# Optimization experiments

Measured on AMD Instinct MI355X. Metric: run time of the kernel, lower is better.

Reference implementation:

```python
import jax, jax.numpy as jnp
import numpy as np

N, D, F, E, K = 8192, 1024, 4096, 8, 2


def setup_inputs() -> dict:
    key = jax.random.key(0)
    ks = jax.random.split(key, 4)
    x = jax.random.normal(ks[0], (N, D), dtype=jnp.float32)
    Wg = jax.random.normal(ks[1], (D, E), dtype=jnp.float32) * 0.02
    W1 = jax.random.normal(ks[2], (E, D, F), dtype=jnp.float32) * 0.02
    b1 = jnp.zeros((E, F), dtype=jnp.float32)
    W2 = jax.random.normal(ks[3], (E, F, D), dtype=jnp.float32) * 0.02
    b2 = jnp.zeros((E, D), dtype=jnp.float32)
    return {"x": x, "Wg": Wg, "W1": W1, "b1": b1, "W2": W2, "b2": b2}


def reference(x, Wg, W1, b1, W2, b2):
    # Top-k softmax gate (TopKGate): pick K experts per token, renormalize.
    logits = x @ Wg                                        # [N, E]
    probs = jax.nn.softmax(logits, axis=-1)
    gate_vals, expert_idx = jax.lax.top_k(probs, K)        # [N, K]
    gate_w = gate_vals / jnp.sum(gate_vals, axis=-1, keepdims=True)

    # Expert FFN (dispatch/combine math): the torch code sorts tokens by expert
    # id, all-to-alls them to the owning rank, applies the local Expert MLP,
    # and combines back weighted by gate_w. The jit-friendly equivalent is to
    # compute every expert's MLP for all tokens and gather the selected rows.
    h = jax.nn.relu(jnp.einsum('nd,edf->enf', x, W1) + b1[:, None, :])  # [E, N, F]
    o = jnp.einsum('enf,efd->end', h, W2) + b2[:, None, :]               # [E, N, D]

    tok = jnp.arange(x.shape[0])
    sel = o[expert_idx, tok[:, None]]                      # [N, K, D]
    y = jnp.sum(gate_w[..., None] * sel, axis=1)           # [N, D]
    return y
```

## Files before the change

kernel.cpp:

```cpp
#include <hip/hip_runtime.h>

#define N_TOK 8192
#define DIM   1024
#define FFN   4096
#define NEXP  8
#define TOPK  2
#define NENT  (N_TOK * TOPK)
#define MAXM  20

using short8   = __attribute__((ext_vector_type(8))) short;
using ushort8v = __attribute__((ext_vector_type(8))) unsigned short;
using floatx4  = __attribute__((ext_vector_type(4))) float;

__device__ __forceinline__ unsigned short f2bf(float f) {
    union { float f; unsigned u; } v; v.f = f;
    unsigned r = v.u + 0x7fffu + ((v.u >> 16) & 1u);
    return (unsigned short)(r >> 16);
}

#define GLOAD_LDS16(gptr, lptr) __builtin_amdgcn_global_load_lds( \
    (__attribute__((address_space(1))) void*)(void*)(gptr),       \
    (__attribute__((address_space(3))) void*)(lptr), 16, 0, 0)


__device__ __forceinline__ void transpose_tile(const float* __restrict__ inp,
                                               unsigned short* __restrict__ outp,
                                               int R, int C, int r0, int c0,
                                               float* __restrict__ tile) {
    int t = threadIdx.x;
    int p = t & 7;
    int trow = t >> 3;
    int w = t >> 6;
#pragma unroll
    for (int i = 0; i < 8; i++) {
        int r = i * 32 + trow;
        float4 v = *(const float4*)&inp[(size_t)(r0 + r) * C + c0 + p * 4];
        int cc = p ^ ((4 * i + w) & 7);
        *(float4*)&tile[r * 32 + cc * 4] = v;
    }
    __syncthreads();
    int c = t >> 3;
    int cbase = ((c >> 2) ^ p) * 4 + (c & 3);
    unsigned short* orow = outp + (size_t)(c0 + c) * R + r0;
#pragma unroll
    for (int j = 0; j < 4; j++) {
        int rb = j * 64 + p * 8;
        ushort8v us;
#pragma unroll
        for (int k = 0; k < 8; k++)
            us[k] = f2bf(tile[(rb + k) * 32 + cbase]);
        *(ushort8v*)&orow[rb] = us;
    }
}


__global__ __launch_bounds__(256) void prep_kernel(
    const float* __restrict__ W1, unsigned short* __restrict__ w1t,
    const float* __restrict__ x, const float* __restrict__ wg,
    unsigned short* __restrict__ xb,
    int* __restrict__ topk_e, float* __restrict__ topk_w,
    int* __restrict__ counts)
{
    __shared__ float tile[8192];
    int bid = blockIdx.x;
    if (bid < 4096) {
        int rt = bid & 3;
        int ct = (bid >> 2) & 127;
        int e  = bid >> 9;
        transpose_tile(W1 + (size_t)e * DIM * FFN, w1t + (size_t)e * DIM * FFN,
                       DIM, FFN, rt * 256, ct * 32, tile);
        return;
    }

    int tid = threadIdx.x;
    int wave = tid >> 6, lane = tid & 63;
    int t = (bid - 4096) * 4 + wave;
    const float* xr = x + (size_t)t * DIM;
    unsigned short* xbr = xb + (size_t)t * DIM;
    float acc[NEXP];
#pragma unroll
    for (int e = 0; e < NEXP; e++) acc[e] = 0.f;
    for (int it = 0; it < DIM / 256; it++) {
        int d = it * 256 + lane * 4;
        float4 xv = *(const float4*)&xr[d];
        ushort4 ub;
        ub.x = f2bf(xv.x); ub.y = f2bf(xv.y); ub.z = f2bf(xv.z); ub.w = f2bf(xv.w);
        *(ushort4*)&xbr[d] = ub;
        const float* wp = wg + (size_t)d * NEXP;
#pragma unroll
        for (int j = 0; j < 4; j++) {
            float xj = (j == 0) ? xv.x : (j == 1) ? xv.y : (j == 2) ? xv.z : xv.w;
            const float4* wr = (const float4*)(wp + j * NEXP);
            float4 w0 = wr[0], w1 = wr[1];
            acc[0] += xj * w0.x; acc[1] += xj * w0.y; acc[2] += xj * w0.z; acc[3] += xj * w0.w;
            acc[4] += xj * w1.x; acc[5] += xj * w1.y; acc[6] += xj * w1.z; acc[7] += xj * w1.w;
        }
    }
#pragma unroll
    for (int e = 0; e < NEXP; e++) {
#pragma unroll
        for (int off = 32; off > 0; off >>= 1) acc[e] += __shfl_xor(acc[e], off);
    }
    if (lane == 0) {
        int e1 = 0; float l1 = acc[0];
        for (int e = 1; e < NEXP; e++) if (acc[e] > l1) { l1 = acc[e]; e1 = e; }
        int e2 = -1; float l2 = -3.4e38f;
        for (int e = 0; e < NEXP; e++) if (e != e1 && acc[e] > l2) { l2 = acc[e]; e2 = e; }
        float w1v = 1.f / (1.f + expf(l2 - l1));
        topk_e[t * 2]     = e1;  topk_e[t * 2 + 1] = e2;
        topk_w[t * 2]     = w1v; topk_w[t * 2 + 1] = 1.f - w1v;
        atomicAdd(&counts[e1], 1);
        atomicAdd(&counts[e2], 1);
    }
}


__global__ __launch_bounds__(256) void scatter_kernel(const int* __restrict__ topk_e,
                                                      const float* __restrict__ topk_w,
                                                      const int* __restrict__ counts,
                                                      int* __restrict__ offs,
                                                      int* __restrict__ cursors,
                                                      int* __restrict__ entry_token,
                                                      float* __restrict__ entry_w,
                                                      float* __restrict__ y) {
    if (blockIdx.x >= 32) {
        float4 z = make_float4(0.f, 0.f, 0.f, 0.f);
        float4* yp = (float4*)y;
        size_t base = (size_t)(blockIdx.x - 32) * 256 + threadIdx.x;
#pragma unroll
        for (int i = 0; i < 16; i++)
            yp[base + (size_t)i * 512 * 256] = z;
        return;
    }
    int off_[NEXP]; int s = 0;
#pragma unroll
    for (int e = 0; e < NEXP; e++) { off_[e] = s; s += counts[e]; }
    if (blockIdx.x == 0 && threadIdx.x == 0) {
#pragma unroll
        for (int e = 0; e < NEXP; e++) offs[e] = off_[e];
        offs[NEXP] = s;
    }
    int t = blockIdx.x * 256 + threadIdx.x;
#pragma unroll
    for (int k = 0; k < TOPK; k++) {
        int e = topk_e[t * 2 + k];
        int pos = off_[e] + atomicAdd(&cursors[e], 1);
        entry_token[pos] = t;
        entry_w[pos] = topk_w[t * 2 + k];
    }
}


union __align__(16) G1Smem {
    struct { unsigned short As[2][4096]; unsigned short Bs[2][4096]; int toks[128]; } g;
    float tile[8192];
};

__global__ __launch_bounds__(256, 3) void gemm1_kernel(
    const unsigned short* __restrict__ xb,
    const unsigned short* __restrict__ w1t,
    const float* __restrict__ b1,
    const int* __restrict__ offs,
    const int* __restrict__ entry_token,
    unsigned short* __restrict__ h,
    const float* __restrict__ W2,
    unsigned short* __restrict__ w2t)
{
    __shared__ G1Smem sm;
    int bid0 = blockIdx.x;
    int bid;
    if (bid0 < 8192) {
        int c = bid0 >> 4, r = bid0 & 15;
        if (r < 8) {
            int tIdx = c * 8 + r;
            int rt = tIdx & 15;
            int ct = (tIdx >> 4) & 31;
            int e  = tIdx >> 9;
            transpose_tile(W2 + (size_t)e * DIM * FFN, w2t + (size_t)e * DIM * FFN,
                           FFN, DIM, rt * 256, ct * 32, sm.tile);
            return;
        }
        bid = c * 8 + (r - 8);
    } else {
        bid = bid0 - 4096;
    }

    int xcd   = bid & 7;
    int inner = bid >> 3;
    int gq    = inner / MAXM;
    int mt    = inner - gq * MAXM;
    int g     = gq * 8 + xcd;
    int e     = g >> 5;
    int nt    = g & 31;
    int base = offs[e];
    int cnt  = offs[e + 1] - base;
    int m0   = mt * 128;
    if (m0 >= cnt) return;
    int f0   = nt * 128;

    auto& As   = sm.g.As;
    auto& Bs   = sm.g.Bs;
    auto& toks = sm.g.toks;

    int tid = threadIdx.x;
    if (tid < 128) {
        int r = m0 + tid;
        toks[tid] = entry_token[base + (r < cnt ? r : 0)];
    }
    __syncthreads();

    int wave = tid >> 6, lane = tid & 63;
    int wm = (wave >> 1) * 64, wn = (wave & 1) * 64;

    int lr = lane >> 2, sl = lane & 3;
    int g0 = (sl ^ ((lr >> 1) & 3)) * 8;
    const unsigned short* aG[2];
    const unsigned short* bG[2];
    int ldsOff[2];
#pragma unroll
    for (int c = 0; c < 2; c++) {
        int row = wave * 32 + c * 16 + lr;
        aG[c] = xb + (size_t)toks[row] * DIM + g0;
        bG[c] = w1t + ((size_t)e * FFN + f0 + row) * DIM + g0;
        ldsOff[c] = (wave * 32 + c * 16) * 32;
    }

    floatx4 acc[4][4];
#pragma unroll
    for (int i = 0; i < 4; i++)
#pragma unroll
        for (int j = 0; j < 4; j++) acc[i][j] = (floatx4)0.f;

    int quad = lane >> 4, rm = lane & 15;
    int slf  = (quad ^ ((rm >> 1) & 3)) * 8;
    int arow = (wm + rm) * 32;
    int brow = (wn + rm) * 32;

#pragma unroll
    for (int c = 0; c < 2; c++) {
        GLOAD_LDS16(aG[c], &As[0][ldsOff[c]]);
        GLOAD_LDS16(bG[c], &Bs[0][ldsOff[c]]);
        aG[c] += 32; bG[c] += 32;
    }

    int cur = 0;
    for (int kk = 0; kk < DIM / 32; kk++) {
        __syncthreads();
        short8 af[4], bfr[4];
#pragma unroll
        for (int mi = 0; mi < 4; mi++) af[mi] = *(const short8*)&As[cur][arow + mi * 512 + slf];
#pragma unroll
        for (int ni = 0; ni < 4; ni++) bfr[ni] = *(const short8*)&Bs[cur][brow + ni * 512 + slf];
        if (kk + 1 < DIM / 32) {
            int nxt = cur ^ 1;
#pragma unroll
            for (int c = 0; c < 2; c++) {
                GLOAD_LDS16(aG[c], &As[nxt][ldsOff[c]]);
                GLOAD_LDS16(bG[c], &Bs[nxt][ldsOff[c]]);
                aG[c] += 32; bG[c] += 32;
            }
        }
#pragma unroll
        for (int mi = 0; mi < 4; mi++)
#pragma unroll
            for (int ni = 0; ni < 4; ni++)
                acc[mi][ni] = __builtin_amdgcn_mfma_f32_16x16x32_bf16(af[mi], bfr[ni], acc[mi][ni], 0, 0, 0);
        cur ^= 1;
    }

#pragma unroll
    for (int mi = 0; mi < 4; mi++) {
        int mbase = wm + mi * 16 + quad * 4;
#pragma unroll
        for (int ni = 0; ni < 4; ni++) {
            int f = f0 + wn + ni * 16 + rm;
            float bias = b1[e * FFN + f];
            floatx4 v = acc[mi][ni];
#pragma unroll
            for (int r = 0; r < 4; r++) {
                int row = m0 + mbase + r;
                if (row < cnt) {
                    float t = v[r] + bias;
                    t = t > 0.f ? t : 0.f;
                    h[(size_t)(base + row) * FFN + f] = f2bf(t);
                }
            }
        }
    }
}


__global__ __launch_bounds__(256, 3) void gemm2_kernel(
    const unsigned short* __restrict__ h,
    const unsigned short* __restrict__ w2t,
    const float* __restrict__ b2,
    const int* __restrict__ offs,
    const int* __restrict__ entry_token,
    const float* __restrict__ entry_w,
    float* __restrict__ y)
{
    int bid  = blockIdx.x;
    int e    = bid & 7;
    int grp  = bid % (8 * MAXM);
    int mt   = grp >> 3;
    int nt   = bid / (8 * MAXM);
    int base = offs[e];
    int cnt  = offs[e + 1] - base;
    int m0   = mt * 128;
    if (m0 >= cnt) return;
    int n0   = nt * 128;

    __shared__ unsigned short As[2][128 * 32];
    __shared__ unsigned short Bs[2][128 * 32];

    int tid = threadIdx.x;
    int wave = tid >> 6, lane = tid & 63;
    int wm = (wave >> 1) * 64, wn = (wave & 1) * 64;

    int lr = lane >> 2, sl = lane & 3;
    int g0 = (sl ^ ((lr >> 1) & 3)) * 8;
    const unsigned short* aG[2];
    const unsigned short* bG[2];
    int ldsOff[2];
#pragma unroll
    for (int c = 0; c < 2; c++) {
        int row = wave * 32 + c * 16 + lr;
        aG[c] = h + (size_t)(base + m0 + row) * FFN + g0;
        bG[c] = w2t + ((size_t)e * DIM + n0 + row) * FFN + g0;
        ldsOff[c] = (wave * 32 + c * 16) * 32;
    }

    floatx4 acc[4][4];
#pragma unroll
    for (int i = 0; i < 4; i++)
#pragma unroll
        for (int j = 0; j < 4; j++) acc[i][j] = (floatx4)0.f;

    int quad = lane >> 4, rm = lane & 15;
    int slf  = (quad ^ ((rm >> 1) & 3)) * 8;
    int arow = (wm + rm) * 32;
    int brow = (wn + rm) * 32;

#pragma unroll
    for (int c = 0; c < 2; c++) {
        GLOAD_LDS16(aG[c], &As[0][ldsOff[c]]);
        GLOAD_LDS16(bG[c], &Bs[0][ldsOff[c]]);
        aG[c] += 32; bG[c] += 32;
    }

    int cur = 0;
    for (int kk = 0; kk < FFN / 32; kk++) {
        __syncthreads();
        short8 af[4], bfr[4];
#pragma unroll
        for (int mi = 0; mi < 4; mi++) af[mi] = *(const short8*)&As[cur][arow + mi * 512 + slf];
#pragma unroll
        for (int ni = 0; ni < 4; ni++) bfr[ni] = *(const short8*)&Bs[cur][brow + ni * 512 + slf];
        if (kk + 1 < FFN / 32) {
            int nxt = cur ^ 1;
#pragma unroll
            for (int c = 0; c < 2; c++) {
                GLOAD_LDS16(aG[c], &As[nxt][ldsOff[c]]);
                GLOAD_LDS16(bG[c], &Bs[nxt][ldsOff[c]]);
                aG[c] += 32; bG[c] += 32;
            }
        }
#pragma unroll
        for (int mi = 0; mi < 4; mi++)
#pragma unroll
            for (int ni = 0; ni < 4; ni++)
                acc[mi][ni] = __builtin_amdgcn_mfma_f32_16x16x32_bf16(af[mi], bfr[ni], acc[mi][ni], 0, 0, 0);
        cur ^= 1;
    }

    float bs[4];
#pragma unroll
    for (int ni = 0; ni < 4; ni++) bs[ni] = b2[e * DIM + n0 + wn + ni * 16 + rm];
#pragma unroll
    for (int mi = 0; mi < 4; mi++) {
        int mbase = wm + mi * 16 + quad * 4;
#pragma unroll
        for (int r = 0; r < 4; r++) {
            int row = m0 + mbase + r;
            if (row < cnt) {
                int tok = entry_token[base + row];
                float w = entry_w[base + row];
                float* yr = y + (size_t)tok * DIM;
#pragma unroll
                for (int ni = 0; ni < 4; ni++) {
                    int n = n0 + wn + ni * 16 + rm;
                    atomicAdd(&yr[n], w * (acc[mi][ni][r] + bs[ni]));
                }
            }
        }
    }
}


extern "C" void kernel_launch(void* const* d_in, const int* in_sizes, int n_in,
                              void* d_out, int out_size, void* d_ws, size_t ws_size,
                              hipStream_t stream) {
    const float* x  = (const float*)d_in[0];
    const float* Wg = (const float*)d_in[1];
    const float* W1 = (const float*)d_in[2];
    const float* b1 = (const float*)d_in[3];
    const float* W2 = (const float*)d_in[4];
    const float* b2 = (const float*)d_in[5];
    float* y = (float*)d_out;

    char* p = (char*)d_ws;
    unsigned short* xb  = (unsigned short*)p; p += (size_t)N_TOK * DIM * 2;
    unsigned short* w1t = (unsigned short*)p; p += (size_t)NEXP * DIM * FFN * 2;
    unsigned short* w2t = (unsigned short*)p; p += (size_t)NEXP * DIM * FFN * 2;
    unsigned short* h   = (unsigned short*)p; p += (size_t)(NENT + 128) * FFN * 2;
    int*   topk_e      = (int*)p;   p += (size_t)N_TOK * TOPK * 4;
    float* topk_w      = (float*)p; p += (size_t)N_TOK * TOPK * 4;
    int*   entry_token = (int*)p;   p += (size_t)NENT * 4;
    float* entry_w     = (float*)p; p += (size_t)NENT * 4;
    int*   counts      = (int*)p;   p += NEXP * 4;
    int*   cursors     = (int*)p;   p += NEXP * 4;
    int*   offs        = (int*)p;   p += (NEXP + 1) * 4;

    hipMemsetAsync(counts, 0, NEXP * 4 * 2, stream);

    prep_kernel<<<4096 + N_TOK / 4, 256, 0, stream>>>(W1, w1t, x, Wg, xb,
                                                      topk_e, topk_w, counts);
    scatter_kernel<<<32 + 512, 256, 0, stream>>>(topk_e, topk_w, counts, offs,
                                                 cursors, entry_token, entry_w, y);
    gemm1_kernel<<<8192 + 1024, 256, 0, stream>>>(
        xb, w1t, b1, offs, entry_token, h, W2, w2t);
    gemm2_kernel<<<NEXP * MAXM * (DIM / 128), 256, 0, stream>>>(h, w2t, b2, offs,
                                                                entry_token, entry_w, y);
}
```

Baseline: 1.079 ms.

## Reshape weight transpose tiles to 128x64 with padded LDS and serialize W2 transpose

The fp32-to-bf16 weight transpose now uses 128x64 tiles staged in LDS with a padded row stride of 68 floats, replacing the XOR-swizzled 256x32 tiles. Each thread now writes contiguous 16-byte chunks, with four threads per output row, instead of eight threads per row. In gemm1, the W2 transpose blocks run as a separate leading range of blocks rather than being interleaved with GEMM tiles, and the grid is sized from the routing constants. This aims to widen global read rows and cut LDS bank conflicts. The risk is that the transpose no longer overlaps with GEMM work in the same dispatch window.

```diff
diff --git a/kernel.cpp b/kernel.cpp
--- a/kernel.cpp
+++ b/kernel.cpp
@@ -28,27 +28,23 @@
                                                int R, int C, int r0, int c0,
                                                float* __restrict__ tile) {
     int t = threadIdx.x;
-    int p = t & 7;
-    int trow = t >> 3;
-    int w = t >> 6;
+    int p = t & 15, q = t >> 4;
 #pragma unroll
     for (int i = 0; i < 8; i++) {
-        int r = i * 32 + trow;
+        int r = i * 16 + q;
         float4 v = *(const float4*)&inp[(size_t)(r0 + r) * C + c0 + p * 4];
-        int cc = p ^ ((4 * i + w) & 7);
-        *(float4*)&tile[r * 32 + cc * 4] = v;
+        *(float4*)&tile[r * 68 + p * 4] = v;
     }
     __syncthreads();
-    int c = t >> 3;
-    int cbase = ((c >> 2) ^ p) * 4 + (c & 3);
+    int c = t >> 2, s = t & 3;
     unsigned short* orow = outp + (size_t)(c0 + c) * R + r0;
 #pragma unroll
     for (int j = 0; j < 4; j++) {
-        int rb = j * 64 + p * 8;
+        int rb = j * 32 + s * 8;
         ushort8v us;
 #pragma unroll
         for (int k = 0; k < 8; k++)
-            us[k] = f2bf(tile[(rb + k) * 32 + cbase]);
+            us[k] = f2bf(tile[(rb + k) * 68 + c]);
         *(ushort8v*)&orow[rb] = us;
     }
 }
@@ -61,14 +57,14 @@
     int* __restrict__ topk_e, float* __restrict__ topk_w,
     int* __restrict__ counts)
 {
-    __shared__ float tile[8192];
+    __shared__ float tile[128 * 68];
     int bid = blockIdx.x;
     if (bid < 4096) {
-        int rt = bid & 3;
-        int ct = (bid >> 2) & 127;
+        int rt = bid & 7;
+        int ct = (bid >> 3) & 63;
         int e  = bid >> 9;
         transpose_tile(W1 + (size_t)e * DIM * FFN, w1t + (size_t)e * DIM * FFN,
-                       DIM, FFN, rt * 256, ct * 32, tile);
+                       DIM, FFN, rt * 128, ct * 64, tile);
         return;
     }
 
@@ -153,7 +149,7 @@
 
 union __align__(16) G1Smem {
     struct { unsigned short As[2][4096]; unsigned short Bs[2][4096]; int toks[128]; } g;
-    float tile[8192];
+    float tile[128 * 68];
 };
 
 __global__ __launch_bounds__(256, 3) void gemm1_kernel(
@@ -168,23 +164,16 @@
 {
     __shared__ G1Smem sm;
     int bid0 = blockIdx.x;
-    int bid;
-    if (bid0 < 8192) {
-        int c = bid0 >> 4, r = bid0 & 15;
-        if (r < 8) {
-            int tIdx = c * 8 + r;
-            int rt = tIdx & 15;
-            int ct = (tIdx >> 4) & 31;
-            int e  = tIdx >> 9;
-            transpose_tile(W2 + (size_t)e * DIM * FFN, w2t + (size_t)e * DIM * FFN,
-                           FFN, DIM, rt * 256, ct * 32, sm.tile);
-            return;
-        }
-        bid = c * 8 + (r - 8);
-    } else {
-        bid = bid0 - 4096;
-    }
-
+    if (bid0 < 4096) {
+        int rt = bid0 & 31;
+        int ct = (bid0 >> 5) & 15;
+        int e  = bid0 >> 9;
+        transpose_tile(W2 + (size_t)e * DIM * FFN, w2t + (size_t)e * DIM * FFN,
+                       FFN, DIM, rt * 128, ct * 64, sm.tile);
+        return;
+    }
+
+    int bid   = bid0 - 4096;
     int xcd   = bid & 7;
     int inner = bid >> 3;
     int gq    = inner / MAXM;
@@ -427,7 +416,7 @@
                                                       topk_e, topk_w, counts);
     scatter_kernel<<<32 + 512, 256, 0, stream>>>(topk_e, topk_w, counts, offs,
                                                  cursors, entry_token, entry_w, y);
-    gemm1_kernel<<<8192 + 1024, 256, 0, stream>>>(
+    gemm1_kernel<<<4096 + NEXP * MAXM * (FFN / 128), 256, 0, stream>>>(
         xb, w1t, b1, offs, entry_token, h, W2, w2t);
     gemm2_kernel<<<NEXP * MAXM * (DIM / 128), 256, 0, stream>>>(h, w2t, b2, offs,
                                                                 entry_token, entry_w, y);
```

Result: faster. 990.1 us (-8.2%).
